# Optimization experiments

Measured on AMD Instinct MI355X. Metric: run time of the kernel, lower is better.

The kernel has to match this reference:

```python
import jax, jax.numpy as jnp
import numpy as np

GROUP_SIZE = 64
BITS = 4
VALS_PER_WORD = 32 // BITS  # 8 nibbles per uint32


def setup_inputs() -> dict:
    key = jax.random.key(0)
    ks = jax.random.split(key, 7)
    B, S, I, O = 4, 2048, 4096, 4096
    G = I // GROUP_SIZE
    x = jax.random.normal(ks[0], (B, S, I), dtype=jnp.float32)
    channel_scale = jax.random.uniform(ks[1], (1, 1, I), dtype=jnp.float32, minval=0.5, maxval=1.5)
    # packed int4 weights: random uint32 words
    qweight = jax.random.randint(ks[2], (O, I // VALS_PER_WORD), 0, 2147483647, dtype=jnp.int32).astype(jnp.uint32)
    q_perm = jax.random.permutation(ks[3], I).astype(jnp.int32)
    scales = jax.random.uniform(ks[4], (O, G), dtype=jnp.float32, minval=0.001, maxval=0.02)
    zeros = jax.random.normal(ks[5], (O, G), dtype=jnp.float32) * 0.05
    bias = jax.random.normal(ks[6], (O,), dtype=jnp.float32) * 0.02
    return {"x": x, "channel_scale": channel_scale, "qweight": qweight,
            "q_perm": q_perm, "scales": scales, "zeros": zeros, "bias": bias}


def _dequantize(qweight, scales, zeros):
    # qweight: (O, I/8) uint32 -> nibbles little-endian within each word
    O, packed = qweight.shape
    shifts = (jnp.arange(VALS_PER_WORD, dtype=jnp.uint32) * BITS)  # (8,)
    wq = (qweight[:, :, None] >> shifts[None, None, :]) & jnp.uint32((1 << BITS) - 1)
    wq = wq.reshape(O, packed * VALS_PER_WORD).astype(jnp.float32)  # (O, I)
    # mlx dequantize: w = wq * scale + bias(zeros), per group of GROUP_SIZE along input dim
    s = jnp.repeat(scales, GROUP_SIZE, axis=1)  # (O, I)
    z = jnp.repeat(zeros, GROUP_SIZE, axis=1)   # (O, I)
    return wq * s + z


def reference(x, channel_scale, qweight, q_perm, scales, zeros, bias):
    # per-channel scale
    x = x * channel_scale
    # optional permute gather along feature axis
    x = jnp.take(x, q_perm, axis=-1)
    # group-wise int4 dequant matmul (transpose=True: out = x @ W^T)
    W = _dequantize(qweight, scales, zeros)  # (O, I)
    out = jnp.einsum('bsi,oi->bso', x, W)
    return out + bias
```

## Files before the change

kernel.cpp:

```cpp
#include <hip/hip_runtime.h>
#include <hip/hip_bf16.h>

typedef unsigned short u16;
typedef unsigned int u32;
typedef unsigned char u8;

#define M_DIM 8192
#define K_DIM 4096
#define N_DIM 4096
#define GROUPS 64

typedef int intx4 __attribute__((ext_vector_type(4)));

__device__ __forceinline__ void gload_lds16(const void* g, void* l) {
  __builtin_amdgcn_global_load_lds(
      (const __attribute__((address_space(1))) void*)g,
      (__attribute__((address_space(3))) void*)l, 16, 0, 0);
}

__device__ __forceinline__ float block_absmax(float amax, float* red) {
#pragma unroll
  for (int off = 32; off; off >>= 1)
    amax = fmaxf(amax, __shfl_xor(amax, off, 64));
  const int wave = threadIdx.x >> 6;
  if ((threadIdx.x & 63) == 0) red[wave] = amax;
  __syncthreads();
  return fmaxf(fmaxf(red[0], red[1]), fmaxf(red[2], red[3]));
}

__device__ __forceinline__ u32 pack4(const float* v, float inv) {
  u32 r = 0;
#pragma unroll
  for (int i = 0; i < 4; ++i) {
    int q = (int)__builtin_rintf(v[i] * inv);
    q = q > 127 ? 127 : (q < -127 ? -127 : q);
    r |= ((u32)(u8)(char)q) << (8 * i);
  }
  return r;
}

__global__ __launch_bounds__(256) void prep_x(
    const float* __restrict__ x, const float* __restrict__ cs,
    u8* __restrict__ xq, float* __restrict__ sx) {
  __shared__ float red[4];
  const size_t m = blockIdx.x;
  const float* xr = x + m * K_DIM;
  const int base = threadIdx.x * 16;
  float v[16];
  float amax = 0.f;
#pragma unroll
  for (int j = 0; j < 4; ++j) {
    float4 xv = *(const float4*)(xr + base + j * 4);
    float4 cv = *(const float4*)(cs + base + j * 4);
    v[j * 4 + 0] = xv.x * cv.x;
    v[j * 4 + 1] = xv.y * cv.y;
    v[j * 4 + 2] = xv.z * cv.z;
    v[j * 4 + 3] = xv.w * cv.w;
#pragma unroll
    for (int i = 0; i < 4; ++i) amax = fmaxf(amax, fabsf(v[j * 4 + i]));
  }
  amax = block_absmax(amax, red);
  amax = fmaxf(amax, 1e-20f);
  const float inv = 127.0f / amax;
  uint4 p;
  p.x = pack4(v + 0, inv);
  p.y = pack4(v + 4, inv);
  p.z = pack4(v + 8, inv);
  p.w = pack4(v + 12, inv);
  *(uint4*)(xq + m * K_DIM + base) = p;
  if (threadIdx.x == 0) sx[m] = amax * (1.0f / 127.0f);
}

__global__ __launch_bounds__(256) void prep_w(
    const u32* __restrict__ qw, const int* __restrict__ perm,
    const float* __restrict__ scales, const float* __restrict__ zeros,
    u8* __restrict__ wq, float* __restrict__ sw) {
  __shared__ float rowbuf[K_DIM];
  __shared__ float red[4];
  const int o = blockIdx.x;
  const u32* qrow = qw + (size_t)o * (K_DIM / 8);
  float amax = 0.f;
#pragma unroll
  for (int it = 0; it < 2; ++it) {
    int t = it * 256 + threadIdx.x;
    u32 q = qrow[t];
    int g = t >> 3;
    float s = scales[o * GROUPS + g];
    float z = zeros[o * GROUPS + g];
#pragma unroll
    for (int n = 0; n < 8; ++n) {
      float v = (float)((q >> (4 * n)) & 15u) * s + z;
      amax = fmaxf(amax, fabsf(v));
      rowbuf[perm[t * 8 + n]] = v;
    }
  }
  __syncthreads();
  amax = block_absmax(amax, red);
  amax = fmaxf(amax, 1e-20f);
  const float inv = 127.0f / amax;
  const int base = threadIdx.x * 16;
  uint4 p;
  p.x = pack4(rowbuf + base + 0, inv);
  p.y = pack4(rowbuf + base + 4, inv);
  p.z = pack4(rowbuf + base + 8, inv);
  p.w = pack4(rowbuf + base + 12, inv);
  *(uint4*)(wq + (size_t)o * K_DIM + base) = p;
  if (threadIdx.x == 0) sw[o] = amax * (1.0f / 127.0f);
}

#define BM 256
#define BN 256
#define BK 64
#define KTILES (K_DIM / BK)

__global__ __launch_bounds__(512, 2) void gemm_i8(
    const u8* __restrict__ A, const u8* __restrict__ B,
    const float* __restrict__ sx, const float* __restrict__ sw,
    const float* __restrict__ bias, float* __restrict__ out) {
  __shared__ __align__(16) u8 As[3][BM * BK];
  __shared__ __align__(16) u8 Bs[3][BN * BK];
  const int tid = threadIdx.x;
  const int lane = tid & 63;
  const int wave = tid >> 6;
  const int wm = wave >> 2;
  const int wn = wave & 3;
  const int q = lane >> 4, lr = lane & 15;
  const int qs = q ^ ((lr >> 1) & 3);
  const int blockN = blockIdx.x * BN;
  const int blockM = blockIdx.y * BM;

  const char* Abase = (const char*)(A + (size_t)blockM * K_DIM);
  const char* Bbase = (const char*)(B + (size_t)blockN * K_DIM);

  const int c0 = tid, c1 = tid + 512;
  const int r0 = c0 >> 2, kc0 = (c0 & 3) ^ ((c0 >> 3) & 3);
  const int r1 = c1 >> 2, kc1 = (c1 & 3) ^ ((c1 >> 3) & 3);

  intx4 acc[8][4];
#pragma unroll
  for (int i = 0; i < 8; ++i)
#pragma unroll
    for (int j = 0; j < 4; ++j) acc[i][j] = (intx4)0;

  auto stage = [&](int t, int b) {
    const size_t koff = (size_t)t * BK;
    gload_lds16(Abase + (size_t)r0 * K_DIM + koff + kc0 * 16, &As[b][c0 * 16]);
    gload_lds16(Abase + (size_t)r1 * K_DIM + koff + kc1 * 16, &As[b][c1 * 16]);
    gload_lds16(Bbase + (size_t)r0 * K_DIM + koff + kc0 * 16, &Bs[b][c0 * 16]);
    gload_lds16(Bbase + (size_t)r1 * K_DIM + koff + kc1 * 16, &Bs[b][c1 * 16]);
  };

  auto compute = [&](int b) {
    intx4 af[8], bf[4];
#pragma unroll
    for (int mi = 0; mi < 8; ++mi)
      af[mi] = *(const intx4*)&As[b][(wm * 128 + mi * 16 + lr) * 64 + qs * 16];
#pragma unroll
    for (int ni = 0; ni < 4; ++ni)
      bf[ni] = *(const intx4*)&Bs[b][(wn * 64 + ni * 16 + lr) * 64 + qs * 16];
    __builtin_amdgcn_s_setprio(1);
#pragma unroll
    for (int mi = 0; mi < 8; ++mi)
#pragma unroll
      for (int ni = 0; ni < 4; ++ni)
        acc[mi][ni] = __builtin_amdgcn_mfma_i32_16x16x64_i8(
            af[mi], bf[ni], acc[mi][ni], 0, 0, 0);
    __builtin_amdgcn_s_setprio(0);
  };

  stage(0, 0);
  stage(1, 1);
  asm volatile("s_waitcnt vmcnt(4)\n\ts_barrier" ::: "memory");

  int bc = 0;
  int bs = 2;
  for (int t = 0; t < KTILES - 2; ++t) {
    stage(t + 2, bs);
    compute(bc);
    asm volatile("s_waitcnt vmcnt(4)\n\ts_barrier" ::: "memory");
    bc = (bc == 2) ? 0 : bc + 1;
    bs = (bs == 2) ? 0 : bs + 1;
  }
  compute(bc);
  asm volatile("s_waitcnt vmcnt(0)\n\ts_barrier" ::: "memory");
  bc = (bc == 2) ? 0 : bc + 1;
  compute(bc);

#pragma unroll
  for (int ni = 0; ni < 4; ++ni) {
    const int col = blockN + wn * 64 + ni * 16 + lr;
    const float swv = sw[col];
    const float bv = bias[col];
#pragma unroll
    for (int mi = 0; mi < 8; ++mi) {
      const int row0 = blockM + wm * 128 + mi * 16 + q * 4;
#pragma unroll
      for (int r = 0; r < 4; ++r) {
        const float s = sx[row0 + r] * swv;
        out[(size_t)(row0 + r) * N_DIM + col] = (float)acc[mi][ni][r] * s + bv;
      }
    }
  }
}

extern "C" void kernel_launch(void* const* d_in, const int* in_sizes, int n_in,
                              void* d_out, int out_size, void* d_ws, size_t ws_size,
                              hipStream_t stream) {
  const float* x      = (const float*)d_in[0];
  const float* cs     = (const float*)d_in[1];
  const u32*   qw     = (const u32*)d_in[2];
  const int*   perm   = (const int*)d_in[3];
  const float* scales = (const float*)d_in[4];
  const float* zeros  = (const float*)d_in[5];
  const float* bias   = (const float*)d_in[6];
  float* out = (float*)d_out;

  u8* xq = (u8*)d_ws;
  u8* wq = xq + (size_t)M_DIM * K_DIM;
  float* sx = (float*)(wq + (size_t)N_DIM * K_DIM);
  float* sw = sx + M_DIM;

  hipLaunchKernelGGL(prep_x, dim3(M_DIM), dim3(256), 0, stream, x, cs, xq, sx);
  hipLaunchKernelGGL(prep_w, dim3(N_DIM), dim3(256), 0, stream,
                     qw, perm, scales, zeros, wq, sw);
  hipLaunchKernelGGL(gemm_i8, dim3(N_DIM / BN, M_DIM / BM), dim3(512), 0,
                     stream, xq, wq, sx, sw, bias, out);
}
```

Baseline: 420.7 us.

## Move permutation gather to activations and interleave prefetch with MFMA phases

```diff
diff --git a/kernel.cpp b/kernel.cpp
--- a/kernel.cpp
+++ b/kernel.cpp
@@ -41,23 +41,60 @@
 
 __global__ __launch_bounds__(256) void prep_x(
     const float* __restrict__ x, const float* __restrict__ cs,
-    u8* __restrict__ xq, float* __restrict__ sx) {
+    const int* __restrict__ perm, u8* __restrict__ xq, float* __restrict__ sx) {
+  __shared__ float row[K_DIM];
   __shared__ float red[4];
   const size_t m = blockIdx.x;
   const float* xr = x + m * K_DIM;
-  const int base = threadIdx.x * 16;
+  const int t = threadIdx.x;
+  float amax = 0.f;
+#pragma unroll
+  for (int j = 0; j < 16; ++j) {
+    const int idx = j * 256 + t;
+    float v = xr[idx] * cs[idx];
+    amax = fmaxf(amax, fabsf(v));
+    row[idx] = v;
+  }
+  amax = block_absmax(amax, red);
+  amax = fmaxf(amax, 1e-20f);
+  const float inv = 127.0f / amax;
+  const int base = t * 16;
+  int4 p0 = *(const int4*)(perm + base + 0);
+  int4 p1 = *(const int4*)(perm + base + 4);
+  int4 p2 = *(const int4*)(perm + base + 8);
+  int4 p3 = *(const int4*)(perm + base + 12);
+  float g[16];
+  g[0]  = row[p0.x]; g[1]  = row[p0.y]; g[2]  = row[p0.z]; g[3]  = row[p0.w];
+  g[4]  = row[p1.x]; g[5]  = row[p1.y]; g[6]  = row[p1.z]; g[7]  = row[p1.w];
+  g[8]  = row[p2.x]; g[9]  = row[p2.y]; g[10] = row[p2.z]; g[11] = row[p2.w];
+  g[12] = row[p3.x]; g[13] = row[p3.y]; g[14] = row[p3.z]; g[15] = row[p3.w];
+  uint4 pk;
+  pk.x = pack4(g + 0, inv);
+  pk.y = pack4(g + 4, inv);
+  pk.z = pack4(g + 8, inv);
+  pk.w = pack4(g + 12, inv);
+  *(uint4*)(xq + m * K_DIM + base) = pk;
+  if (t == 0) sx[m] = amax * (1.0f / 127.0f);
+}
+
+__global__ __launch_bounds__(256) void prep_w(
+    const u32* __restrict__ qw,
+    const float* __restrict__ scales, const float* __restrict__ zeros,
+    u8* __restrict__ wq, float* __restrict__ sw) {
+  __shared__ float red[4];
+  const int o = blockIdx.x;
+  const u32* qrow = qw + (size_t)o * (K_DIM / 8);
+  const int t = threadIdx.x;
+  const float s = scales[o * GROUPS + (t >> 2)];
+  const float z = zeros[o * GROUPS + (t >> 2)];
+  uint2 w = *(const uint2*)(qrow + 2 * t);
   float v[16];
   float amax = 0.f;
 #pragma unroll
-  for (int j = 0; j < 4; ++j) {
-    float4 xv = *(const float4*)(xr + base + j * 4);
-    float4 cv = *(const float4*)(cs + base + j * 4);
-    v[j * 4 + 0] = xv.x * cv.x;
-    v[j * 4 + 1] = xv.y * cv.y;
-    v[j * 4 + 2] = xv.z * cv.z;
-    v[j * 4 + 3] = xv.w * cv.w;
-#pragma unroll
-    for (int i = 0; i < 4; ++i) amax = fmaxf(amax, fabsf(v[j * 4 + i]));
+  for (int n = 0; n < 8; ++n) {
+    v[n]     = (float)((w.x >> (4 * n)) & 15u) * s + z;
+    v[8 + n] = (float)((w.y >> (4 * n)) & 15u) * s + z;
+    amax = fmaxf(amax, fmaxf(fabsf(v[n]), fabsf(v[8 + n])));
   }
   amax = block_absmax(amax, red);
   amax = fmaxf(amax, 1e-20f);
@@ -67,45 +104,8 @@
   p.y = pack4(v + 4, inv);
   p.z = pack4(v + 8, inv);
   p.w = pack4(v + 12, inv);
-  *(uint4*)(xq + m * K_DIM + base) = p;
-  if (threadIdx.x == 0) sx[m] = amax * (1.0f / 127.0f);
-}
-
-__global__ __launch_bounds__(256) void prep_w(
-    const u32* __restrict__ qw, const int* __restrict__ perm,
-    const float* __restrict__ scales, const float* __restrict__ zeros,
-    u8* __restrict__ wq, float* __restrict__ sw) {
-  __shared__ float rowbuf[K_DIM];
-  __shared__ float red[4];
-  const int o = blockIdx.x;
-  const u32* qrow = qw + (size_t)o * (K_DIM / 8);
-  float amax = 0.f;
-#pragma unroll
-  for (int it = 0; it < 2; ++it) {
-    int t = it * 256 + threadIdx.x;
-    u32 q = qrow[t];
-    int g = t >> 3;
-    float s = scales[o * GROUPS + g];
-    float z = zeros[o * GROUPS + g];
-#pragma unroll
-    for (int n = 0; n < 8; ++n) {
-      float v = (float)((q >> (4 * n)) & 15u) * s + z;
-      amax = fmaxf(amax, fabsf(v));
-      rowbuf[perm[t * 8 + n]] = v;
-    }
-  }
-  __syncthreads();
-  amax = block_absmax(amax, red);
-  amax = fmaxf(amax, 1e-20f);
-  const float inv = 127.0f / amax;
-  const int base = threadIdx.x * 16;
-  uint4 p;
-  p.x = pack4(rowbuf + base + 0, inv);
-  p.y = pack4(rowbuf + base + 4, inv);
-  p.z = pack4(rowbuf + base + 8, inv);
-  p.w = pack4(rowbuf + base + 12, inv);
-  *(uint4*)(wq + (size_t)o * K_DIM + base) = p;
-  if (threadIdx.x == 0) sw[o] = amax * (1.0f / 127.0f);
+  *(uint4*)(wq + (size_t)o * K_DIM + t * 16) = p;
+  if (t == 0) sw[o] = amax * (1.0f / 127.0f);
 }
 
 #define BM 256
@@ -133,8 +133,14 @@
   const char* Bbase = (const char*)(B + (size_t)blockN * K_DIM);
 
   const int c0 = tid, c1 = tid + 512;
-  const int r0 = c0 >> 2, kc0 = (c0 & 3) ^ ((c0 >> 3) & 3);
-  const int r1 = c1 >> 2, kc1 = (c1 & 3) ^ ((c1 >> 3) & 3);
+  const int kc0 = (c0 & 3) ^ ((c0 >> 3) & 3);
+  const int kc1 = (c1 & 3) ^ ((c1 >> 3) & 3);
+  const size_t gOff0 = (size_t)(c0 >> 2) * K_DIM + kc0 * 16;
+  const size_t gOff1 = (size_t)(c1 >> 2) * K_DIM + kc1 * 16;
+  const int dOff0 = c0 * 16, dOff1 = c1 * 16;
+
+  const int aoff = (wm * 128 + lr) * 64 + qs * 16;
+  const int boff = (wn * 64 + lr) * 64 + qs * 16;
 
   intx4 acc[8][4];
 #pragma unroll
@@ -142,49 +148,78 @@
 #pragma unroll
     for (int j = 0; j < 4; ++j) acc[i][j] = (intx4)0;
 
-  auto stage = [&](int t, int b) {
-    const size_t koff = (size_t)t * BK;
-    gload_lds16(Abase + (size_t)r0 * K_DIM + koff + kc0 * 16, &As[b][c0 * 16]);
-    gload_lds16(Abase + (size_t)r1 * K_DIM + koff + kc1 * 16, &As[b][c1 * 16]);
-    gload_lds16(Bbase + (size_t)r0 * K_DIM + koff + kc0 * 16, &Bs[b][c0 * 16]);
-    gload_lds16(Bbase + (size_t)r1 * K_DIM + koff + kc1 * 16, &Bs[b][c1 * 16]);
-  };
-
-  auto compute = [&](int b) {
-    intx4 af[8], bf[4];
-#pragma unroll
-    for (int mi = 0; mi < 8; ++mi)
-      af[mi] = *(const intx4*)&As[b][(wm * 128 + mi * 16 + lr) * 64 + qs * 16];
-#pragma unroll
-    for (int ni = 0; ni < 4; ++ni)
-      bf[ni] = *(const intx4*)&Bs[b][(wn * 64 + ni * 16 + lr) * 64 + qs * 16];
-    __builtin_amdgcn_s_setprio(1);
-#pragma unroll
-    for (int mi = 0; mi < 8; ++mi)
-#pragma unroll
-      for (int ni = 0; ni < 4; ++ni)
-        acc[mi][ni] = __builtin_amdgcn_mfma_i32_16x16x64_i8(
-            af[mi], bf[ni], acc[mi][ni], 0, 0, 0);
-    __builtin_amdgcn_s_setprio(0);
-  };
-
-  stage(0, 0);
-  stage(1, 1);
-  asm volatile("s_waitcnt vmcnt(4)\n\ts_barrier" ::: "memory");
-
-  int bc = 0;
-  int bs = 2;
-  for (int t = 0; t < KTILES - 2; ++t) {
-    stage(t + 2, bs);
-    compute(bc);
-    asm volatile("s_waitcnt vmcnt(4)\n\ts_barrier" ::: "memory");
+  gload_lds16(Abase + gOff0, &As[0][dOff0]);
+  gload_lds16(Abase + gOff1, &As[0][dOff1]);
+  gload_lds16(Bbase + gOff0, &Bs[0][dOff0]);
+  gload_lds16(Bbase + gOff1, &Bs[0][dOff1]);
+  gload_lds16(Abase + gOff0 + BK, &As[1][dOff0]);
+  gload_lds16(Abase + gOff1 + BK, &As[1][dOff1]);
+  gload_lds16(Bbase + gOff0 + BK, &Bs[1][dOff0]);
+  gload_lds16(Bbase + gOff1 + BK, &Bs[1][dOff1]);
+  asm volatile("s_waitcnt vmcnt(4)" ::: "memory");
+  asm volatile("s_barrier" ::: "memory");
+
+  int bc = 0, bs = 2;
+  for (int t = 0; t < KTILES; ++t) {
+    const u8* Ab = &As[bc][0];
+    const u8* Bb = &Bs[bc][0];
+    u8* Aw = &As[bs][0];
+    u8* Bw = &Bs[bs][0];
+    const size_t koff2 = (size_t)(t + 2) * BK;
+    const bool pf = (t + 2 < KTILES);
+    intx4 bf[4], a0, a1;
+
+#define MFMA8(MI0, MI1)                                                     \
+  __builtin_amdgcn_s_setprio(1);                                            \
+  _Pragma("unroll") for (int ni = 0; ni < 4; ++ni)                          \
+      acc[MI0][ni] = __builtin_amdgcn_mfma_i32_16x16x64_i8(                 \
+          a0, bf[ni], acc[MI0][ni], 0, 0, 0);                               \
+  _Pragma("unroll") for (int ni = 0; ni < 4; ++ni)                          \
+      acc[MI1][ni] = __builtin_amdgcn_mfma_i32_16x16x64_i8(                 \
+          a1, bf[ni], acc[MI1][ni], 0, 0, 0);                               \
+  __builtin_amdgcn_s_setprio(0);
+
+    bf[0] = *(const intx4*)(Bb + boff + 0 * 1024);
+    bf[1] = *(const intx4*)(Bb + boff + 1 * 1024);
+    bf[2] = *(const intx4*)(Bb + boff + 2 * 1024);
+    bf[3] = *(const intx4*)(Bb + boff + 3 * 1024);
+    a0 = *(const intx4*)(Ab + aoff + 0 * 1024);
+    a1 = *(const intx4*)(Ab + aoff + 1 * 1024);
+    if (pf) gload_lds16(Abase + gOff0 + koff2, Aw + dOff0);
+    asm volatile("s_barrier" ::: "memory");
+    MFMA8(0, 1)
+    asm volatile("s_barrier" ::: "memory");
+
+    a0 = *(const intx4*)(Ab + aoff + 2 * 1024);
+    a1 = *(const intx4*)(Ab + aoff + 3 * 1024);
+    if (pf) gload_lds16(Abase + gOff1 + koff2, Aw + dOff1);
+    asm volatile("s_barrier" ::: "memory");
+    MFMA8(2, 3)
+    asm volatile("s_barrier" ::: "memory");
+
+    a0 = *(const intx4*)(Ab + aoff + 4 * 1024);
+    a1 = *(const intx4*)(Ab + aoff + 5 * 1024);
+    if (pf) gload_lds16(Bbase + gOff0 + koff2, Bw + dOff0);
+    asm volatile("s_barrier" ::: "memory");
+    MFMA8(4, 5)
+    asm volatile("s_barrier" ::: "memory");
+
+    a0 = *(const intx4*)(Ab + aoff + 6 * 1024);
+    a1 = *(const intx4*)(Ab + aoff + 7 * 1024);
+    if (pf) gload_lds16(Bbase + gOff1 + koff2, Bw + dOff1);
+    asm volatile("s_barrier" ::: "memory");
+    MFMA8(6, 7)
+    if (t < KTILES - 2) {
+      asm volatile("s_waitcnt vmcnt(4)" ::: "memory");
+    } else if (t == KTILES - 2) {
+      asm volatile("s_waitcnt vmcnt(0)" ::: "memory");
+    }
+    if (t < KTILES - 1) asm volatile("s_barrier" ::: "memory");
+
     bc = (bc == 2) ? 0 : bc + 1;
     bs = (bs == 2) ? 0 : bs + 1;
-  }
-  compute(bc);
-  asm volatile("s_waitcnt vmcnt(0)\n\ts_barrier" ::: "memory");
-  bc = (bc == 2) ? 0 : bc + 1;
-  compute(bc);
+#undef MFMA8
+  }
 
 #pragma unroll
   for (int ni = 0; ni < 4; ++ni) {
@@ -220,9 +255,9 @@
   float* sx = (float*)(wq + (size_t)N_DIM * K_DIM);
   float* sw = sx + M_DIM;
 
-  hipLaunchKernelGGL(prep_x, dim3(M_DIM), dim3(256), 0, stream, x, cs, xq, sx);
+  hipLaunchKernelGGL(prep_x, dim3(M_DIM), dim3(256), 0, stream, x, cs, perm, xq, sx);
   hipLaunchKernelGGL(prep_w, dim3(N_DIM), dim3(256), 0, stream,
-                     qw, perm, scales, zeros, wq, sw);
+                     qw, scales, zeros, wq, sw);
   hipLaunchKernelGGL(gemm_i8, dim3(N_DIM / BN, M_DIM / BM), dim3(512), 0,
                      stream, xq, wq, sx, sw, bias, out);
 }
```

New measurement: 414.4 us. About the same (-1.5%).
